# Kernel tuning notes

Hardware: AMD Instinct MI355X
Metric: run time of the kernel (lower is better)

Reference implementation:

```python
import jax, jax.numpy as jnp
import numpy as np

N_NODES = 50000
N_EDGES = 800000
HEADS = 8
DIM = 32
NEG_SLOPE = 0.2


def setup_inputs() -> dict:
    key = jax.random.key(0)
    k1, k2, k3, k4, k5 = jax.random.split(key, 5)
    feat = jax.random.normal(k1, (N_NODES, HEADS * DIM), dtype=jnp.float32)
    attn_l = jax.random.normal(k2, (1, HEADS, DIM), dtype=jnp.float32)
    attn_r = jax.random.normal(k3, (1, HEADS, DIM), dtype=jnp.float32)
    src_idx = jax.random.randint(k4, (N_EDGES,), 0, N_NODES, dtype=jnp.int32)
    dst_idx = jnp.sort(jax.random.randint(k5, (N_EDGES,), 0, N_NODES, dtype=jnp.int32))
    return {"feat": feat, "attn_l": attn_l, "attn_r": attn_r,
            "src_idx": src_idx, "dst_idx": dst_idx}


def reference(feat, attn_l, attn_r, src_idx, dst_idx):
    # [N, H, D] node features
    h = feat.reshape(-1, HEADS, DIM)
    n = h.shape[0]
    # per-node attention logits: [N, H]
    el = jnp.sum(h * attn_l, axis=-1)
    er = jnp.sum(h * attn_r, axis=-1)
    # edge scores e = leaky_relu(el[u] + er[v]): [E, H]
    e = jax.nn.leaky_relu(el[src_idx] + er[dst_idx], negative_slope=NEG_SLOPE)
    # segment softmax over incoming edges of each dst node
    e_max = jax.ops.segment_max(e, dst_idx, num_segments=n)          # [N, H]
    e_exp = jnp.exp(e - e_max[dst_idx])                              # [E, H]
    denom = jax.ops.segment_sum(e_exp, dst_idx, num_segments=n)     # [N, H]
    a = e_exp / denom[dst_idx]                                      # [E, H]
    # weighted scatter-sum aggregation: sum_{u in N(v)} a_uv * h_u
    m = h[src_idx] * a[:, :, None]                                  # [E, H, D]
    out = jax.ops.segment_sum(m, dst_idx, num_segments=n)           # [N, H, D]
    return out
```

## Files before the change

kernel.cpp:

```cpp
#include <hip/hip_runtime.h>
#include <hip/hip_fp16.h>
#include <math.h>

#define HEADS 8
#define DIM 32
#define NEG_SLOPE 0.2f

__device__ inline float2 u2f2(unsigned int u) {
    __half2 h = __builtin_bit_cast(__half2, u);
    return __half22float2(h);
}

__global__ void gat_logits_conv_kernel(const float* __restrict__ feat,
                                       const float* __restrict__ attn_l,
                                       const float* __restrict__ attn_r,
                                       float* __restrict__ el,
                                       float* __restrict__ er,
                                       __half2* __restrict__ feat_h2,
                                       int nh_total) {
    int idx = blockIdx.x * blockDim.x + threadIdx.x;
    if (idx >= nh_total) return;
    int h = idx & (HEADS - 1);
    const float4* f  = reinterpret_cast<const float4*>(feat + (size_t)idx * DIM);
    const float4* al = reinterpret_cast<const float4*>(attn_l + h * DIM);
    const float4* ar = reinterpret_cast<const float4*>(attn_r + h * DIM);
    __half2* oh = feat_h2 + (size_t)idx * (DIM / 2);
    float sl = 0.f, sr = 0.f;
#pragma unroll
    for (int i = 0; i < DIM / 4; ++i) {
        float4 v = f[i];
        float4 a = al[i];
        float4 b = ar[i];
        sl += v.x * a.x + v.y * a.y + v.z * a.z + v.w * a.w;
        sr += v.x * b.x + v.y * b.y + v.z * b.z + v.w * b.w;
        oh[2 * i]     = __floats2half2_rn(v.x, v.y);
        oh[2 * i + 1] = __floats2half2_rn(v.z, v.w);
    }
    el[idx] = sl;
    er[idx] = sr;
}

__global__ void build_rowptr_kernel(const int* __restrict__ dst,
                                    int* __restrict__ rowptr,
                                    int n_edges, int n_nodes) {
    int e = blockIdx.x * blockDim.x + threadIdx.x;
    if (e >= n_edges) return;
    int d = dst[e];
    int prev = (e > 0) ? dst[e - 1] : -1;
    for (int v = prev + 1; v <= d; ++v) rowptr[v] = e;
    if (e == n_edges - 1) {
        for (int v = d + 1; v <= n_nodes; ++v) rowptr[v] = n_edges;
    }
}

__global__ __launch_bounds__(256) void gat_aggregate_kernel(
    const uint2* __restrict__ feat_h,
    const float* __restrict__ el,
    const float* __restrict__ er,
    const int* __restrict__ src_idx,
    const int* __restrict__ rowptr,
    float4* __restrict__ out4,
    int n_nodes) {
    int v = (blockIdx.x * blockDim.x + threadIdx.x) >> 6;
    if (v >= n_nodes) return;
    int lane = threadIdx.x & 63;
    int h = lane >> 3;

    int start = rowptr[v];
    int end   = rowptr[v + 1];

    size_t obase = (size_t)v * 64 + lane;
    if (start == end) {
        out4[obase] = make_float4(0.f, 0.f, 0.f, 0.f);
        return;
    }

    float er_vh = er[v * HEADS + h];

    float denom = 0.f;
    float4 accA = make_float4(0.f, 0.f, 0.f, 0.f);
    float4 accB = make_float4(0.f, 0.f, 0.f, 0.f);

    for (int e = start; e < end; e += 8) {
        int   idx[8];
        uint2 fr[8];
        float w[8];
#pragma unroll
        for (int i = 0; i < 8; ++i) {
            int ee = (e + i < end) ? (e + i) : (end - 1);
            idx[i] = src_idx[ee];
        }
#pragma unroll
        for (int i = 0; i < 8; ++i) {
            fr[i] = feat_h[(size_t)idx[i] * 64 + lane];
        }
#pragma unroll
        for (int i = 0; i < 8; ++i) {
            float s = el[(size_t)idx[i] * HEADS + h] + er_vh;
            s = s > 0.f ? s : NEG_SLOPE * s;
            float ww = __expf(s);
            w[i] = (e + i < end) ? ww : 0.f;
        }
#pragma unroll
        for (int i = 0; i < 8; ++i) {
            float2 lo = u2f2(fr[i].x);
            float2 hi = u2f2(fr[i].y);
            float ww = w[i];
            denom += ww;
            if (i & 1) {
                accB.x += ww * lo.x; accB.y += ww * lo.y;
                accB.z += ww * hi.x; accB.w += ww * hi.y;
            } else {
                accA.x += ww * lo.x; accA.y += ww * lo.y;
                accA.z += ww * hi.x; accA.w += ww * hi.y;
            }
        }
    }
    float inv = 1.f / denom;
    float4 r;
    r.x = (accA.x + accB.x) * inv;
    r.y = (accA.y + accB.y) * inv;
    r.z = (accA.z + accB.z) * inv;
    r.w = (accA.w + accB.w) * inv;
    out4[obase] = r;
}

extern "C" void kernel_launch(void* const* d_in, const int* in_sizes, int n_in,
                              void* d_out, int out_size, void* d_ws, size_t ws_size,
                              hipStream_t stream) {
    const float* feat   = (const float*)d_in[0];
    const float* attn_l = (const float*)d_in[1];
    const float* attn_r = (const float*)d_in[2];
    const int*   src    = (const int*)d_in[3];
    const int*   dst    = (const int*)d_in[4];
    float* out = (float*)d_out;

    int n_edges = in_sizes[3];
    int n_nodes = out_size / (HEADS * DIM);
    int nh = n_nodes * HEADS;

    char* ws = (char*)d_ws;
    float* el = (float*)ws;                       ws += (size_t)nh * 4;
    float* er = (float*)ws;                       ws += (size_t)nh * 4;
    int* rowptr = (int*)ws;                       ws += (size_t)(n_nodes + 1) * 4;
    ws = (char*)(((uintptr_t)ws + 15) & ~(uintptr_t)15);
    __half2* feat_h2 = (__half2*)ws;

    hipLaunchKernelGGL(gat_logits_conv_kernel,
                       dim3((nh + 255) / 256), dim3(256), 0, stream,
                       feat, attn_l, attn_r, el, er, feat_h2, nh);

    hipLaunchKernelGGL(build_rowptr_kernel,
                       dim3((n_edges + 255) / 256), dim3(256), 0, stream,
                       dst, rowptr, n_edges, n_nodes);

    int blocks = (n_nodes + 3) / 4;
    hipLaunchKernelGGL(gat_aggregate_kernel,
                       dim3(blocks), dim3(256), 0, stream,
                       (const uint2*)feat_h2, el, er, src, rowptr, (float4*)out,
                       n_nodes);
}
```

Measured before the change: 111.4 us.

## Process two nodes per wavefront with 16-byte gathers and coalesce logits kernel

The aggregation kernel now assigns two destination nodes per 64-lane wavefront, with each lane gathering 16 bytes (8 fp16 values) per source edge instead of 8, which halves the number of gather instructions per edge. The half-waves loop to the longer of the two degrees, so degree imbalance adds some idle iterations. The logits/conversion kernel is rewritten to one wavefront per node with coalesced float4 loads and shuffle reductions, replacing strided per-thread 128-byte reads.

```diff
diff --git a/kernel.cpp b/kernel.cpp
--- a/kernel.cpp
+++ b/kernel.cpp
@@ -11,33 +11,39 @@
     return __half22float2(h);
 }
 
-__global__ void gat_logits_conv_kernel(const float* __restrict__ feat,
-                                       const float* __restrict__ attn_l,
-                                       const float* __restrict__ attn_r,
-                                       float* __restrict__ el,
-                                       float* __restrict__ er,
-                                       __half2* __restrict__ feat_h2,
-                                       int nh_total) {
-    int idx = blockIdx.x * blockDim.x + threadIdx.x;
-    if (idx >= nh_total) return;
-    int h = idx & (HEADS - 1);
-    const float4* f  = reinterpret_cast<const float4*>(feat + (size_t)idx * DIM);
-    const float4* al = reinterpret_cast<const float4*>(attn_l + h * DIM);
-    const float4* ar = reinterpret_cast<const float4*>(attn_r + h * DIM);
-    __half2* oh = feat_h2 + (size_t)idx * (DIM / 2);
-    float sl = 0.f, sr = 0.f;
+__global__ __launch_bounds__(256) void gat_logits_conv_kernel(
+    const float4* __restrict__ feat4,
+    const float4* __restrict__ attn_l4,
+    const float4* __restrict__ attn_r4,
+    float* __restrict__ el,
+    float* __restrict__ er,
+    uint2* __restrict__ feat_h2,
+    int n_nodes) {
+    int wid = (blockIdx.x * blockDim.x + threadIdx.x) >> 6;
+    if (wid >= n_nodes) return;
+    int lane = threadIdx.x & 63;
+    int h = lane >> 3;
+    int q = lane & 7;
+
+    float4 al = attn_l4[lane];
+    float4 ar = attn_r4[lane];
+    float4 v  = feat4[(size_t)wid * 64 + lane];
+
+    float sl = v.x * al.x + v.y * al.y + v.z * al.z + v.w * al.w;
+    float sr = v.x * ar.x + v.y * ar.y + v.z * ar.z + v.w * ar.w;
 #pragma unroll
-    for (int i = 0; i < DIM / 4; ++i) {
-        float4 v = f[i];
-        float4 a = al[i];
-        float4 b = ar[i];
-        sl += v.x * a.x + v.y * a.y + v.z * a.z + v.w * a.w;
-        sr += v.x * b.x + v.y * b.y + v.z * b.z + v.w * b.w;
-        oh[2 * i]     = __floats2half2_rn(v.x, v.y);
-        oh[2 * i + 1] = __floats2half2_rn(v.z, v.w);
+    for (int off = 1; off < 8; off <<= 1) {
+        sl += __shfl_xor(sl, off, 64);
+        sr += __shfl_xor(sr, off, 64);
     }
-    el[idx] = sl;
-    er[idx] = sr;
+    if (q == 0) {
+        el[wid * HEADS + h] = sl;
+        er[wid * HEADS + h] = sr;
+    }
+    uint2 o;
+    o.x = __builtin_bit_cast(unsigned int, __floats2half2_rn(v.x, v.y));
+    o.y = __builtin_bit_cast(unsigned int, __floats2half2_rn(v.z, v.w));
+    feat_h2[(size_t)wid * 64 + lane] = o;
 }
 
 __global__ void build_rowptr_kernel(const int* __restrict__ dst,
@@ -54,75 +60,85 @@
 }
 
 __global__ __launch_bounds__(256) void gat_aggregate_kernel(
-    const uint2* __restrict__ feat_h,
+    const uint4* __restrict__ feat_h4,
     const float* __restrict__ el,
     const float* __restrict__ er,
     const int* __restrict__ src_idx,
     const int* __restrict__ rowptr,
     float4* __restrict__ out4,
     int n_nodes) {
-    int v = (blockIdx.x * blockDim.x + threadIdx.x) >> 6;
-    if (v >= n_nodes) return;
+    int wid = (blockIdx.x * blockDim.x + threadIdx.x) >> 6;
     int lane = threadIdx.x & 63;
-    int h = lane >> 3;
+    int s = lane & 31;
+    int h = s >> 2;
+    int v = wid * 2 + (lane >> 5);
+    bool valid = v < n_nodes;
+    int vv = valid ? v : (n_nodes - 1);
 
-    int start = rowptr[v];
-    int end   = rowptr[v + 1];
+    int start = rowptr[vv];
+    int end   = rowptr[vv + 1];
+    if (!valid) end = start;
+    int len = end - start;
 
-    size_t obase = (size_t)v * 64 + lane;
-    if (start == end) {
-        out4[obase] = make_float4(0.f, 0.f, 0.f, 0.f);
-        return;
-    }
+    float er_vh = er[vv * HEADS + h];
 
-    float er_vh = er[v * HEADS + h];
+    int len0 = __shfl(len, 0, 64);
+    int len1 = __shfl(len, 32, 64);
+    int maxlen = len0 > len1 ? len0 : len1;
 
-    float denom = 0.f;
-    float4 accA = make_float4(0.f, 0.f, 0.f, 0.f);
-    float4 accB = make_float4(0.f, 0.f, 0.f, 0.f);
+    float denomA = 0.f, denomB = 0.f;
+    float acc[8];
+#pragma unroll
+    for (int j = 0; j < 8; ++j) acc[j] = 0.f;
 
-    for (int e = start; e < end; e += 8) {
+    for (int k = 0; k < maxlen; k += 8) {
         int   idx[8];
-        uint2 fr[8];
+        uint4 fr[8];
         float w[8];
 #pragma unroll
         for (int i = 0; i < 8; ++i) {
-            int ee = (e + i < end) ? (e + i) : (end - 1);
+            int e = start + k + i;
+            int ee = e < end ? e : (end - 1);
+            ee = ee < 0 ? 0 : ee;
             idx[i] = src_idx[ee];
         }
 #pragma unroll
         for (int i = 0; i < 8; ++i) {
-            fr[i] = feat_h[(size_t)idx[i] * 64 + lane];
+            fr[i] = feat_h4[(size_t)idx[i] * 32 + s];
         }
 #pragma unroll
         for (int i = 0; i < 8; ++i) {
-            float s = el[(size_t)idx[i] * HEADS + h] + er_vh;
-            s = s > 0.f ? s : NEG_SLOPE * s;
-            float ww = __expf(s);
-            w[i] = (e + i < end) ? ww : 0.f;
+            float sc = el[(size_t)idx[i] * HEADS + h] + er_vh;
+            sc = sc > 0.f ? sc : NEG_SLOPE * sc;
+            float ww = __expf(sc);
+            w[i] = (k + i < len) ? ww : 0.f;
         }
 #pragma unroll
         for (int i = 0; i < 8; ++i) {
-            float2 lo = u2f2(fr[i].x);
-            float2 hi = u2f2(fr[i].y);
             float ww = w[i];
-            denom += ww;
-            if (i & 1) {
-                accB.x += ww * lo.x; accB.y += ww * lo.y;
-                accB.z += ww * hi.x; accB.w += ww * hi.y;
-            } else {
-                accA.x += ww * lo.x; accA.y += ww * lo.y;
-                accA.z += ww * hi.x; accA.w += ww * hi.y;
-            }
+            if (i & 1) denomB += ww; else denomA += ww;
+            float2 p0 = u2f2(fr[i].x);
+            float2 p1 = u2f2(fr[i].y);
+            float2 p2 = u2f2(fr[i].z);
+            float2 p3 = u2f2(fr[i].w);
+            acc[0] += ww * p0.x; acc[1] += ww * p0.y;
+            acc[2] += ww * p1.x; acc[3] += ww * p1.y;
+            acc[4] += ww * p2.x; acc[5] += ww * p2.y;
+            acc[6] += ww * p3.x; acc[7] += ww * p3.y;
         }
     }
-    float inv = 1.f / denom;
-    float4 r;
-    r.x = (accA.x + accB.x) * inv;
-    r.y = (accA.y + accB.y) * inv;
-    r.z = (accA.z + accB.z) * inv;
-    r.w = (accA.w + accB.w) * inv;
-    out4[obase] = r;
+    if (valid) {
+        float denom = denomA + denomB;
+        float inv = denom > 0.f ? 1.f / denom : 0.f;
+        float4 r0, r1;
+        r0.x = acc[0] * inv; r0.y = acc[1] * inv;
+        r0.z = acc[2] * inv; r0.w = acc[3] * inv;
+        r1.x = acc[4] * inv; r1.y = acc[5] * inv;
+        r1.z = acc[6] * inv; r1.w = acc[7] * inv;
+        size_t ob = (size_t)v * 64 + (size_t)s * 2;
+        out4[ob]     = r0;
+        out4[ob + 1] = r1;
+    }
 }
 
 extern "C" void kernel_launch(void* const* d_in, const int* in_sizes, int n_in,
@@ -144,19 +160,20 @@
     float* er = (float*)ws;                       ws += (size_t)nh * 4;
     int* rowptr = (int*)ws;                       ws += (size_t)(n_nodes + 1) * 4;
     ws = (char*)(((uintptr_t)ws + 15) & ~(uintptr_t)15);
-    __half2* feat_h2 = (__half2*)ws;
+    uint2* feat_h2 = (uint2*)ws;
 
     hipLaunchKernelGGL(gat_logits_conv_kernel,
-                       dim3((nh + 255) / 256), dim3(256), 0, stream,
-                       feat, attn_l, attn_r, el, er, feat_h2, nh);
+                       dim3((n_nodes + 3) / 4), dim3(256), 0, stream,
+                       (const float4*)feat, (const float4*)attn_l,
+                       (const float4*)attn_r, el, er, feat_h2, n_nodes);
 
     hipLaunchKernelGGL(build_rowptr_kernel,
                        dim3((n_edges + 255) / 256), dim3(256), 0, stream,
                        dst, rowptr, n_edges, n_nodes);
 
-    int blocks = (n_nodes + 3) / 4;
+    int blocks = (n_nodes + 7) / 8;
     hipLaunchKernelGGL(gat_aggregate_kernel,
                        dim3(blocks), dim3(256), 0, stream,
-                       (const uint2*)feat_h2, el, er, src, rowptr, (float4*)out,
+                       (const uint4*)feat_h2, el, er, src, rowptr, (float4*)out,
                        n_nodes);
 }
```

After: 100.3 us. 1.11x faster.
